# Performance work log

Measured on AMD Instinct MI355X. Metric: run time of the kernel, lower is better.

## Reference

```python
import jax, jax.numpy as jnp
import numpy as np

B, N, F = 16, 256, 64
H = 64  # MLP hidden width


def setup_inputs() -> dict:
    key = jax.random.key(0)
    k_h, k_w1, k_w2 = jax.random.split(key, 3)
    hidden_state = jax.random.normal(k_h, (B, N, F), dtype=jnp.float32)
    # nn.init.normal_(weight, 0.0, 0.01); bias = 0
    w1 = jax.random.normal(k_w1, (H, 2 * F), dtype=jnp.float32) * 0.01  # Linear(128, 64)
    b1 = jnp.zeros((H,), dtype=jnp.float32)
    w2 = jax.random.normal(k_w2, (1, H), dtype=jnp.float32) * 0.01  # Linear(64, 1)
    b2 = jnp.zeros((1,), dtype=jnp.float32)
    return {"hidden_state": hidden_state, "w1": w1, "b1": b1, "w2": w2, "b2": b2}


def reference(hidden_state, w1, b1, w2, b2):
    # hidden_state: [B, N, F]. Pair (i, j) feature = cat(h_i, h_j) -> MLP -> sigmoid.
    # Split first linear: cat(h_i, h_j) @ W1^T == h_i @ W1a^T + h_j @ W1b^T.
    Bsz, Nn, Fd = hidden_state.shape
    w1a, w1b = w1[:, :Fd], w1[:, Fd:]                      # [H, F] each
    a = jnp.einsum('bnf,hf->bnh', hidden_state, w1a)       # [B, N, H] (i-part)
    c = jnp.einsum('bnf,hf->bnh', hidden_state, w1b)       # [B, N, H] (j-part)
    z = jax.nn.relu(a[:, :, None, :] + c[:, None, :, :] + b1)  # [B, N, N, H]
    logits = jnp.einsum('bijh,oh->bijo', z, w2)[..., 0] + b2[0]  # [B, N, N]
    adj = jax.nn.sigmoid(logits)
    # Diagonal entries are never overwritten -> stay 1.
    eye = jnp.eye(Nn, dtype=adj.dtype)
    return adj * (1.0 - eye) + eye
```

## Files before the change

kernel.cpp:

```cpp
#include <hip/hip_runtime.h>
#include <hip/hip_bf16.h>
#include <hip/hip_fp16.h>


#define Nn 256
#define Fd 64
#define Hd 64

typedef _Float16 h2v    __attribute__((ext_vector_type(2)));
typedef __fp16   fp16x2 __attribute__((ext_vector_type(2)));
typedef _Float16 f16x8  __attribute__((ext_vector_type(8)));
typedef float    f32x4  __attribute__((ext_vector_type(4)));
union H2   { h2v v; fp16x2 p; unsigned int u; };
union U4F8 { uint4 u; f16x8 v; };
union HS1  { _Float16 h; unsigned short s; };

__global__ __launch_bounds__(512) void fused_kernel(
    const float* __restrict__ hs, const float* __restrict__ w1,
    const float* __restrict__ b1, const float* __restrict__ w2,
    const float* __restrict__ b2, float* __restrict__ out) {
  __shared__ uint2 w1s[64][32];
  __shared__ uint2 hsI[64][16];
  __shared__ uint2 hsJ[64][16];
  __shared__ uint4 aT[64][8];
  __shared__ uint4 cT[64][8];
  __shared__ unsigned int w2h[32];

  const int t  = threadIdx.x;
  const int b  = blockIdx.z;
  const int i0 = blockIdx.y * 64;
  const int j0 = blockIdx.x * 64;

  {
    const float4* w14 = (const float4*)w1;
#pragma unroll
    for (int p = 0; p < 4; ++p) {
      const int k4 = p * 512 + t;
      const int r = k4 >> 5, col4 = k4 & 31;
      const float4 v = w14[k4];
      H2 lo, hi;
      lo.p = __builtin_amdgcn_cvt_pkrtz(v.x, v.y);
      hi.p = __builtin_amdgcn_cvt_pkrtz(v.z, v.w);
      const int cc = col4 >> 1, hf = col4 & 1;
      w1s[r][((cc ^ (r & 15)) << 1) | hf] = make_uint2(lo.u, hi.u);
    }
  }
  {
    const float4* hi4 = (const float4*)(hs + (size_t)(b * Nn + i0) * Fd);
    const float4* hj4 = (const float4*)(hs + (size_t)(b * Nn + j0) * Fd);
#pragma unroll
    for (int p = 0; p < 2; ++p) {
      const int k4 = p * 512 + t;
      const int r = k4 >> 4, col4 = k4 & 15;
      const int cc = col4 >> 1, hf = col4 & 1;
      const int idx = ((cc ^ (r & 7)) << 1) | hf;
      {
        const float4 v = hi4[k4];
        H2 lo, hi_;
        lo.p  = __builtin_amdgcn_cvt_pkrtz(v.x, v.y);
        hi_.p = __builtin_amdgcn_cvt_pkrtz(v.z, v.w);
        hsI[r][idx] = make_uint2(lo.u, hi_.u);
      }
      {
        const float4 v = hj4[k4];
        H2 lo, hi_;
        lo.p  = __builtin_amdgcn_cvt_pkrtz(v.x, v.y);
        hi_.p = __builtin_amdgcn_cvt_pkrtz(v.z, v.w);
        hsJ[r][idx] = make_uint2(lo.u, hi_.u);
      }
    }
  }
  if (t < 32) {
    H2 wv2;
    wv2.v = (h2v){(_Float16)w2[2 * t], (_Float16)w2[2 * t + 1]};
    w2h[t] = wv2.u;
  }
  __syncthreads();

  {
    const int l   = t & 63;
    const int w   = t >> 6;
    const bool isA = (w < 4);
    const int wv  = w & 3;
    const int l15 = l & 15, l4 = l >> 4;
    const int mrow = wv * 16 + l15;

    const uint2 (*hsX)[16] = isA ? hsI : hsJ;
    const int cbase = isA ? 0 : 8;

    f32x4 acc1[4] = {{0,0,0,0},{0,0,0,0},{0,0,0,0},{0,0,0,0}};

#pragma unroll
    for (int s = 0; s < 2; ++s) {
      U4F8 af;
      af.u = ((const uint4*)&hsX[mrow][0])[(s * 4 + l4) ^ (mrow & 7)];
#pragma unroll
      for (int nt = 0; nt < 4; ++nt) {
        const int rh = nt * 16 + l15;
        U4F8 bf;
        bf.u = ((const uint4*)&w1s[rh][0])[(cbase + s * 4 + l4) ^ (rh & 15)];
        acc1[nt] = __builtin_amdgcn_mfma_f32_16x16x32_f16(af.v, bf.v, acc1[nt], 0, 0, 0);
      }
    }

    unsigned short* dTh = isA ? (unsigned short*)aT : (unsigned short*)cT;
#pragma unroll
    for (int nt = 0; nt < 4; ++nt) {
      const int n = nt * 16 + l15;
      const float bval = isA ? b1[n] : 0.f;
      const int chunk = n >> 3, pos = n & 7;
#pragma unroll
      for (int i = 0; i < 4; ++i) {
        const int row = wv * 16 + l4 * 4 + i;
        const int sw = chunk ^ ((row >> 2) & 7);
        HS1 x; x.h = (_Float16)(acc1[nt][i] + bval);
        dTh[row * 64 + sw * 8 + pos] = x.s;
      }
    }
  }
  __syncthreads();

  const int jt  = t & 15;
  const int it2 = t >> 4;
  const int ib  = it2 * 2;
  const int jb  = jt * 4;
  const int sa  = (it2 >> 1) & 7;
  const int sc  = jt & 7;

  const uint4* w2q = (const uint4*)w2h;

  float acc[2][4] = {{0.f}};

#pragma unroll 2
  for (int h8 = 0; h8 < 8; ++h8) {
    const uint4 wwu = w2q[h8];
    uint4 av[2], cv[4];
#pragma unroll
    for (int u = 0; u < 2; ++u) av[u] = aT[ib + u][h8 ^ sa];
#pragma unroll
    for (int v = 0; v < 4; ++v) cv[v] = cT[jb + v][h8 ^ sc];

#pragma unroll
    for (int u = 0; u < 2; ++u) {
      const unsigned au4[4] = {av[u].x, av[u].y, av[u].z, av[u].w};
#pragma unroll
      for (int v = 0; v < 4; ++v) {
        const unsigned cu4[4] = {cv[v].x, cv[v].y, cv[v].z, cv[v].w};
        const unsigned wu4[4] = {wwu.x, wwu.y, wwu.z, wwu.w};
#pragma unroll
        for (int m = 0; m < 4; ++m) {
          H2 za, zc, zw;
          za.u = au4[m]; zc.u = cu4[m]; zw.u = wu4[m];
          h2v z = __builtin_elementwise_max(za.v + zc.v, (h2v)(_Float16)0);
#if __has_builtin(__builtin_amdgcn_fdot2)
          acc[u][v] = __builtin_amdgcn_fdot2(z, zw.v, acc[u][v], false);
#else
          acc[u][v] = fmaf((float)z.x, (float)zw.v.x, acc[u][v]);
          acc[u][v] = fmaf((float)z.y, (float)zw.v.y, acc[u][v]);
#endif
        }
      }
    }
  }

  const float bias2 = b2[0];
#pragma unroll
  for (int u = 0; u < 2; ++u) {
    const int i = i0 + ib + u;
    float4 o;
    o.x = (i == j0 + jb + 0) ? 1.0f : 1.f / (1.f + __expf(-(acc[u][0] + bias2)));
    o.y = (i == j0 + jb + 1) ? 1.0f : 1.f / (1.f + __expf(-(acc[u][1] + bias2)));
    o.z = (i == j0 + jb + 2) ? 1.0f : 1.f / (1.f + __expf(-(acc[u][2] + bias2)));
    o.w = (i == j0 + jb + 3) ? 1.0f : 1.f / (1.f + __expf(-(acc[u][3] + bias2)));
    ((float4*)(out + (size_t)(b * Nn + i) * Nn + j0))[jt] = o;
  }
}

extern "C" void kernel_launch(void* const* d_in, const int* in_sizes, int n_in,
                              void* d_out, int out_size, void* d_ws, size_t ws_size,
                              hipStream_t stream) {
  const float* hs = (const float*)d_in[0];
  const float* w1 = (const float*)d_in[1];
  const float* b1 = (const float*)d_in[2];
  const float* w2 = (const float*)d_in[3];
  const float* b2 = (const float*)d_in[4];
  float* out = (float*)d_out;

  dim3 grid(Nn / 64, Nn / 64, 16);
  fused_kernel<<<grid, 512, 0, stream>>>(hs, w1, b1, w2, b2, out);
}
```

Measured before the change: 12.06 us.

## Shrink pair tiles to 32x32 with 256-thread blocks for more CTAs

```diff
diff --git a/kernel.cpp b/kernel.cpp
--- a/kernel.cpp
+++ b/kernel.cpp
@@ -15,27 +15,27 @@
 union U4F8 { uint4 u; f16x8 v; };
 union HS1  { _Float16 h; unsigned short s; };
 
-__global__ __launch_bounds__(512) void fused_kernel(
+__global__ __launch_bounds__(256) void fused_kernel(
     const float* __restrict__ hs, const float* __restrict__ w1,
     const float* __restrict__ b1, const float* __restrict__ w2,
     const float* __restrict__ b2, float* __restrict__ out) {
   __shared__ uint2 w1s[64][32];
-  __shared__ uint2 hsI[64][16];
-  __shared__ uint2 hsJ[64][16];
-  __shared__ uint4 aT[64][8];
-  __shared__ uint4 cT[64][8];
+  __shared__ uint2 hsI[32][16];
+  __shared__ uint2 hsJ[32][16];
+  __shared__ uint4 aT[32][8];
+  __shared__ uint4 cT[32][8];
   __shared__ unsigned int w2h[32];
 
   const int t  = threadIdx.x;
   const int b  = blockIdx.z;
-  const int i0 = blockIdx.y * 64;
-  const int j0 = blockIdx.x * 64;
+  const int i0 = blockIdx.y * 32;
+  const int j0 = blockIdx.x * 32;
 
   {
     const float4* w14 = (const float4*)w1;
 #pragma unroll
-    for (int p = 0; p < 4; ++p) {
-      const int k4 = p * 512 + t;
+    for (int p = 0; p < 8; ++p) {
+      const int k4 = p * 256 + t;
       const int r = k4 >> 5, col4 = k4 & 31;
       const float4 v = w14[k4];
       H2 lo, hi;
@@ -50,7 +50,7 @@
     const float4* hj4 = (const float4*)(hs + (size_t)(b * Nn + j0) * Fd);
 #pragma unroll
     for (int p = 0; p < 2; ++p) {
-      const int k4 = p * 512 + t;
+      const int k4 = p * 256 + t;
       const int r = k4 >> 4, col4 = k4 & 15;
       const int cc = col4 >> 1, hf = col4 & 1;
       const int idx = ((cc ^ (r & 7)) << 1) | hf;
@@ -80,8 +80,8 @@
   {
     const int l   = t & 63;
     const int w   = t >> 6;
-    const bool isA = (w < 4);
-    const int wv  = w & 3;
+    const bool isA = (w < 2);
+    const int wv  = w & 1;
     const int l15 = l & 15, l4 = l >> 4;
     const int mrow = wv * 16 + l15;
 
@@ -120,58 +120,52 @@
   }
   __syncthreads();
 
-  const int jt  = t & 15;
-  const int it2 = t >> 4;
-  const int ib  = it2 * 2;
-  const int jb  = jt * 4;
-  const int sa  = (it2 >> 1) & 7;
-  const int sc  = jt & 7;
+  const int jt = t & 7;
+  const int it = t >> 3;
+  const int jb = jt * 4;
+  const int sa = (it >> 2) & 7;
+  const int sc = jt;
 
   const uint4* w2q = (const uint4*)w2h;
 
-  float acc[2][4] = {{0.f}};
+  float acc[4] = {0.f, 0.f, 0.f, 0.f};
 
 #pragma unroll 2
   for (int h8 = 0; h8 < 8; ++h8) {
     const uint4 wwu = w2q[h8];
-    uint4 av[2], cv[4];
-#pragma unroll
-    for (int u = 0; u < 2; ++u) av[u] = aT[ib + u][h8 ^ sa];
+    const uint4 av = aT[it][h8 ^ sa];
+    uint4 cv[4];
 #pragma unroll
     for (int v = 0; v < 4; ++v) cv[v] = cT[jb + v][h8 ^ sc];
 
+    const unsigned au4[4] = {av.x, av.y, av.z, av.w};
+    const unsigned wu4[4] = {wwu.x, wwu.y, wwu.z, wwu.w};
 #pragma unroll
-    for (int u = 0; u < 2; ++u) {
-      const unsigned au4[4] = {av[u].x, av[u].y, av[u].z, av[u].w};
+    for (int v = 0; v < 4; ++v) {
+      const unsigned cu4[4] = {cv[v].x, cv[v].y, cv[v].z, cv[v].w};
 #pragma unroll
-      for (int v = 0; v < 4; ++v) {
-        const unsigned cu4[4] = {cv[v].x, cv[v].y, cv[v].z, cv[v].w};
-        const unsigned wu4[4] = {wwu.x, wwu.y, wwu.z, wwu.w};
-#pragma unroll
-        for (int m = 0; m < 4; ++m) {
-          H2 za, zc, zw;
-          za.u = au4[m]; zc.u = cu4[m]; zw.u = wu4[m];
-          h2v z = __builtin_elementwise_max(za.v + zc.v, (h2v)(_Float16)0);
+      for (int m = 0; m < 4; ++m) {
+        H2 za, zc, zw;
+        za.u = au4[m]; zc.u = cu4[m]; zw.u = wu4[m];
+        h2v z = __builtin_elementwise_max(za.v + zc.v, (h2v)(_Float16)0);
 #if __has_builtin(__builtin_amdgcn_fdot2)
-          acc[u][v] = __builtin_amdgcn_fdot2(z, zw.v, acc[u][v], false);
+        acc[v] = __builtin_amdgcn_fdot2(z, zw.v, acc[v], false);
 #else
-          acc[u][v] = fmaf((float)z.x, (float)zw.v.x, acc[u][v]);
-          acc[u][v] = fmaf((float)z.y, (float)zw.v.y, acc[u][v]);
+        acc[v] = fmaf((float)z.x, (float)zw.v.x, acc[v]);
+        acc[v] = fmaf((float)z.y, (float)zw.v.y, acc[v]);
 #endif
-        }
       }
     }
   }
 
   const float bias2 = b2[0];
-#pragma unroll
-  for (int u = 0; u < 2; ++u) {
-    const int i = i0 + ib + u;
+  {
+    const int i = i0 + it;
     float4 o;
-    o.x = (i == j0 + jb + 0) ? 1.0f : 1.f / (1.f + __expf(-(acc[u][0] + bias2)));
-    o.y = (i == j0 + jb + 1) ? 1.0f : 1.f / (1.f + __expf(-(acc[u][1] + bias2)));
-    o.z = (i == j0 + jb + 2) ? 1.0f : 1.f / (1.f + __expf(-(acc[u][2] + bias2)));
-    o.w = (i == j0 + jb + 3) ? 1.0f : 1.f / (1.f + __expf(-(acc[u][3] + bias2)));
+    o.x = (i == j0 + jb + 0) ? 1.0f : 1.f / (1.f + __expf(-(acc[0] + bias2)));
+    o.y = (i == j0 + jb + 1) ? 1.0f : 1.f / (1.f + __expf(-(acc[1] + bias2)));
+    o.z = (i == j0 + jb + 2) ? 1.0f : 1.f / (1.f + __expf(-(acc[2] + bias2)));
+    o.w = (i == j0 + jb + 3) ? 1.0f : 1.f / (1.f + __expf(-(acc[3] + bias2)));
     ((float4*)(out + (size_t)(b * Nn + i) * Nn + j0))[jt] = o;
   }
 }
@@ -186,6 +180,6 @@
   const float* b2 = (const float*)d_in[4];
   float* out = (float*)d_out;
 
-  dim3 grid(Nn / 64, Nn / 64, 16);
-  fused_kernel<<<grid, 512, 0, stream>>>(hs, w1, b1, w2, b2, out);
+  dim3 grid(Nn / 32, Nn / 32, 16);
+  fused_kernel<<<grid, 256, 0, stream>>>(hs, w1, b1, w2, b2, out);
 }
```

After: 12.88 us. 1.07x slower.
